# Kernel optimization log

Measured on AMD Instinct MI355X. Metric: run time of the kernel, lower is better.

The kernel has to match this reference:

```python
import jax, jax.numpy as jnp
import numpy as np


def setup_inputs() -> dict:
    key = jax.random.key(0)
    k1, k2 = jax.random.split(key, 2)
    N, H, W, FIN = 64, 64, 64, 64
    FH, FW, FOUT = 4, 4, 128
    L = (H // FH) * (W // FW)  # 256 output locations (stride == kernel)
    X = jax.random.normal(k1, (N, H, W, FIN), dtype=jnp.float32)
    # 'alexnet' init: normal(0, 0.01), unshared per-location filters
    filters = 0.01 * jax.random.normal(k2, (1, L, FH, FW, FIN, FOUT), dtype=jnp.float32)
    bias = jnp.zeros((FOUT,), dtype=jnp.float32)  # bias init value 0.0
    return {"X": X, "filters": filters, "bias": bias}


def reference(X, filters, bias):
    N, H, W, C = X.shape
    _, L, fh, fw, fin, fout = filters.shape
    rows, cols = H // fh, W // fw
    # image_to_patches (stride==kernel branch): non-overlapping patch extraction
    # patches[n, r*cols+c, i, j, ch] = X[n, r*fh+i, c*fw+j, ch]
    patches = X.reshape(N, rows, fh, cols, fw, C)
    patches = patches.transpose(0, 1, 3, 2, 4, 5).reshape(N, L, fh, fw, C)
    # broadcast-multiply + reduce_sum over (fh, fw, fin) == per-location GEMM
    Z = jnp.einsum('nlijc,lijcf->nlf', patches, filters[0]) + bias
    Z = Z.reshape(N, rows, cols, fout)
    return jax.nn.relu(Z)
```

## Files before the change

kernel.cpp:

```cpp
#include <hip/hip_runtime.h>


typedef __bf16 bf16x8 __attribute__((ext_vector_type(8)));
typedef float f32x4 __attribute__((ext_vector_type(4)));

#define SBP 140

__device__ __forceinline__ unsigned pack2(float a, float b) {
  __bf16 lo = (__bf16)a, hi = (__bf16)b;
  return (unsigned)__builtin_bit_cast(unsigned short, lo) |
         ((unsigned)__builtin_bit_cast(unsigned short, hi) << 16);
}

__global__ __launch_bounds__(512) void bioconv_full(
    const float* __restrict__ X, const float* __restrict__ Fw,
    const float* __restrict__ bias, float* __restrict__ out) {
  const int bx = blockIdx.x;
  const int l = (bx & 7) * 32 + (bx >> 3);
  const int r = l >> 4, c = l & 15;

  const int t = threadIdx.x;
  const int wave = t >> 6, lane = t & 63;
  const int q = lane >> 4, nl = lane & 15;
  const int m0 = (wave >> 1) * 16;
  const int n0 = (wave & 1) * 64;

  __shared__ __align__(16) unsigned short As[2][64 * 128];
  __shared__ __align__(16) unsigned Bs[2][64 * SBP];

  const float* gA = X + r * 16384 + c * 256;
  const float* gB = Fw + (size_t)l * 131072;

  float2 vA[8];
  float4 vB0[4], vB1[4];

  auto loadA = [&](int s) {
    const int off = (s >> 1) * 4096 + (s & 1) * 128 + 2 * lane;
#pragma unroll
    for (int m = 0; m < 8; ++m) {
      const int n = m * 8 + wave;
      vA[m] = *(const float2*)(gA + (size_t)n * 262144 + off);
    }
  };
  auto loadB = [&](int s) {
    const float* base = gB + s * 16384 + 4 * (lane & 31);
#pragma unroll
    for (int m = 0; m < 4; ++m) {
      const int kp = wave * 8 + m * 2 + (lane >> 5);
      vB0[m] = *(const float4*)(base + kp * 256);
      vB1[m] = *(const float4*)(base + kp * 256 + 128);
    }
  };
  auto writeA = [&](int buf) {
    unsigned* base = (unsigned*)&As[buf][0];
#pragma unroll
    for (int m = 0; m < 8; ++m) {
      const int n = m * 8 + wave;
      base[n * 64 + (lane ^ ((n & 7) << 2))] = pack2(vA[m].x, vA[m].y);
    }
  };
  auto writeB = [&](int buf) {
    unsigned* bw = (unsigned*)&Bs[buf][0] + 4 * (lane & 31);
#pragma unroll
    for (int m = 0; m < 4; ++m) {
      const int kp = wave * 8 + m * 2 + (lane >> 5);
      uint4 v;
      v.x = pack2(vB0[m].x, vB1[m].x);
      v.y = pack2(vB0[m].y, vB1[m].y);
      v.z = pack2(vB0[m].z, vB1[m].z);
      v.w = pack2(vB0[m].w, vB1[m].w);
      *(uint4*)(bw + kp * SBP) = v;
    }
  };

  f32x4 acc[4];
#pragma unroll
  for (int fb = 0; fb < 4; ++fb) acc[fb] = (f32x4){0.f, 0.f, 0.f, 0.f};

  auto compute = [&](int buf) {
#pragma unroll
    for (int kk = 0; kk < 4; ++kk) {
      const unsigned short* ap =
          &As[buf][(m0 + nl) * 128 + ((kk * 32 + q * 8) ^ ((nl & 7) << 3))];
      bf16x8 af = *(const bf16x8*)ap;
      const unsigned* bp = (const unsigned*)&Bs[buf][0] + (kk * 16 + q * 4) * SBP + n0 + nl;
#pragma unroll
      for (int fb = 0; fb < 4; ++fb) {
        const unsigned* b = bp + fb * 16;
        uint4 v;
        v.x = b[0];
        v.y = b[SBP];
        v.z = b[2 * SBP];
        v.w = b[3 * SBP];
        bf16x8 bfr = __builtin_bit_cast(bf16x8, v);
        acc[fb] = __builtin_amdgcn_mfma_f32_16x16x32_bf16(af, bfr, acc[fb], 0, 0, 0);
      }
    }
  };

  loadA(0);
  loadB(0);
  writeA(0);
  writeB(0);
  loadA(1);
  loadB(1);
#pragma unroll
  for (int s = 0; s < 8; ++s) {
    asm volatile("s_waitcnt lgkmcnt(0)" ::: "memory");
    __builtin_amdgcn_s_barrier();
    __builtin_amdgcn_sched_barrier(0);
    compute(s & 1);
    if (s + 1 < 8) {
      writeA((s + 1) & 1);
      writeB((s + 1) & 1);
    }
    if (s + 2 < 8) {
      loadA(s + 2);
      loadB(s + 2);
    }
  }

#pragma unroll
  for (int fb = 0; fb < 4; ++fb) {
    const int f = n0 + fb * 16 + nl;
    const float bv = bias[f];
    float* ob = out + (size_t)l * 128 + f;
#pragma unroll
    for (int v = 0; v < 4; ++v) {
      const int row = m0 + q * 4 + v;
      ob[(size_t)row * 32768] = fmaxf(acc[fb][v] + bv, 0.f);
    }
  }
}

extern "C" void kernel_launch(void* const* d_in, const int* in_sizes, int n_in,
                              void* d_out, int out_size, void* d_ws, size_t ws_size,
                              hipStream_t stream) {
  const float* X = (const float*)d_in[0];
  const float* Fw = (const float*)d_in[1];
  const float* bias = (const float*)d_in[2];
  float* out = (float*)d_out;
  bioconv_full<<<256, 512, 0, stream>>>(X, Fw, bias, out);
}
```

Before: 241.9 us.

## Stream fp32 tiles into LDS via direct global-to-LDS loads with triple buffering

Replaces the register-staged load/convert/write path with global_load_lds DMA that copies fp32 tiles of X and filters straight into LDS, using XOR swizzles and a three-stage buffer ring with vmcnt-based waits. The bf16 conversion moves into the compute loop, done when fragments are read from LDS. This is meant to cut register pressure and VALU/LDS-write work in the load phase and to overlap memory better. In exchange it doubles LDS footprint per stage (fp32 instead of bf16), uses more LDS reads and scalar B reads, and repeats the conversion per wave.

```diff
diff --git a/kernel.cpp b/kernel.cpp
--- a/kernel.cpp
+++ b/kernel.cpp
@@ -4,15 +4,27 @@
 typedef __bf16 bf16x8 __attribute__((ext_vector_type(8)));
 typedef float f32x4 __attribute__((ext_vector_type(4)));
 
-#define SBP 140
-
 __device__ __forceinline__ unsigned pack2(float a, float b) {
   __bf16 lo = (__bf16)a, hi = (__bf16)b;
   return (unsigned)__builtin_bit_cast(unsigned short, lo) |
          ((unsigned)__builtin_bit_cast(unsigned short, hi) << 16);
 }
+__device__ __forceinline__ bf16x8 cvt8(float4 lo, float4 hi) {
+  uint4 v;
+  v.x = pack2(lo.x, lo.y);
+  v.y = pack2(lo.z, lo.w);
+  v.z = pack2(hi.x, hi.y);
+  v.w = pack2(hi.z, hi.w);
+  return __builtin_bit_cast(bf16x8, v);
+}
 
-__global__ __launch_bounds__(512) void bioconv_full(
+__device__ __forceinline__ void gl2lds16(const float* g, float* l) {
+  __builtin_amdgcn_global_load_lds(
+      (const __attribute__((address_space(1))) void*)g,
+      (__attribute__((address_space(3))) void*)l, 16, 0, 0);
+}
+
+__global__ __launch_bounds__(512) void bioconv_dma(
     const float* __restrict__ X, const float* __restrict__ Fw,
     const float* __restrict__ bias, float* __restrict__ out) {
   const int bx = blockIdx.x;
@@ -25,51 +37,33 @@
   const int m0 = (wave >> 1) * 16;
   const int n0 = (wave & 1) * 64;
 
-  __shared__ __align__(16) unsigned short As[2][64 * 128];
-  __shared__ __align__(16) unsigned Bs[2][64 * SBP];
+  __shared__ __align__(16) float Als[3][64 * 64];
+  __shared__ __align__(16) float Bls[3][64 * 128];
 
   const float* gA = X + r * 16384 + c * 256;
   const float* gB = Fw + (size_t)l * 131072;
 
-  float2 vA[8];
-  float4 vB0[4], vB1[4];
+  const int arow_lo = lane >> 4;
+  const int achk = lane & 15;
+  const int brow_lo = lane >> 5;
+  const int bchk = lane & 31;
 
-  auto loadA = [&](int s) {
-    const int off = (s >> 1) * 4096 + (s & 1) * 128 + 2 * lane;
+  auto issueA = [&](int s, int buf) {
 #pragma unroll
-    for (int m = 0; m < 8; ++m) {
-      const int n = m * 8 + wave;
-      vA[m] = *(const float2*)(gA + (size_t)n * 262144 + off);
+    for (int j = 0; j < 2; ++j) {
+      const int row = wave * 8 + j * 4 + arow_lo;
+      const int cg = achk ^ (row & 7);
+      const float* g = gA + (size_t)row * 262144 + (s >> 2) * 4096 + (s & 3) * 64 + cg * 4;
+      gl2lds16(g, &Als[buf][(wave * 8 + j * 4) * 64]);
     }
   };
-  auto loadB = [&](int s) {
-    const float* base = gB + s * 16384 + 4 * (lane & 31);
+  auto issueB = [&](int s, int buf) {
 #pragma unroll
-    for (int m = 0; m < 4; ++m) {
-      const int kp = wave * 8 + m * 2 + (lane >> 5);
-      vB0[m] = *(const float4*)(base + kp * 256);
-      vB1[m] = *(const float4*)(base + kp * 256 + 128);
-    }
-  };
-  auto writeA = [&](int buf) {
-    unsigned* base = (unsigned*)&As[buf][0];
-#pragma unroll
-    for (int m = 0; m < 8; ++m) {
-      const int n = m * 8 + wave;
-      base[n * 64 + (lane ^ ((n & 7) << 2))] = pack2(vA[m].x, vA[m].y);
-    }
-  };
-  auto writeB = [&](int buf) {
-    unsigned* bw = (unsigned*)&Bs[buf][0] + 4 * (lane & 31);
-#pragma unroll
-    for (int m = 0; m < 4; ++m) {
-      const int kp = wave * 8 + m * 2 + (lane >> 5);
-      uint4 v;
-      v.x = pack2(vB0[m].x, vB1[m].x);
-      v.y = pack2(vB0[m].y, vB1[m].y);
-      v.z = pack2(vB0[m].z, vB1[m].z);
-      v.w = pack2(vB0[m].w, vB1[m].w);
-      *(uint4*)(bw + kp * SBP) = v;
+    for (int i = 0; i < 4; ++i) {
+      const int row = i * 16 + wave * 2 + brow_lo;
+      const int cswz = bchk ^ (((row >> 3) & 3) << 2);
+      const float* g = gB + (size_t)(s * 64 + row) * 128 + cswz * 4;
+      gl2lds16(g, &Bls[buf][(i * 16 + wave * 2) * 128]);
     }
   };
 
@@ -78,46 +72,46 @@
   for (int fb = 0; fb < 4; ++fb) acc[fb] = (f32x4){0.f, 0.f, 0.f, 0.f};
 
   auto compute = [&](int buf) {
+    const float* Ab = &Als[buf][0];
+    const float* Bb = &Bls[buf][0];
 #pragma unroll
-    for (int kk = 0; kk < 4; ++kk) {
-      const unsigned short* ap =
-          &As[buf][(m0 + nl) * 128 + ((kk * 32 + q * 8) ^ ((nl & 7) << 3))];
-      bf16x8 af = *(const bf16x8*)ap;
-      const unsigned* bp = (const unsigned*)&Bs[buf][0] + (kk * 16 + q * 4) * SBP + n0 + nl;
+    for (int kk = 0; kk < 2; ++kk) {
+      const int cg = kk * 8 + q * 2;
+      const int w0 = (m0 + nl) * 64 + ((cg + 0) ^ (nl & 7)) * 4;
+      const int w1 = (m0 + nl) * 64 + ((cg + 1) ^ (nl & 7)) * 4;
+      float4 a0 = *(const float4*)(Ab + w0);
+      float4 a1 = *(const float4*)(Ab + w1);
+      bf16x8 af = cvt8(a0, a1);
 #pragma unroll
       for (int fb = 0; fb < 4; ++fb) {
-        const unsigned* b = bp + fb * 16;
-        uint4 v;
-        v.x = b[0];
-        v.y = b[SBP];
-        v.z = b[2 * SBP];
-        v.w = b[3 * SBP];
-        bf16x8 bfr = __builtin_bit_cast(bf16x8, v);
+        const int fw = (n0 + fb * 16 + nl) ^ (q << 4);
+        const float* bp = Bb + (kk * 32 + q * 8) * 128 + fw;
+        float b0 = bp[0 * 128], b1 = bp[1 * 128], b2 = bp[2 * 128], b3 = bp[3 * 128];
+        float b4 = bp[4 * 128], b5 = bp[5 * 128], b6 = bp[6 * 128], b7 = bp[7 * 128];
+        bf16x8 bfr = cvt8(make_float4(b0, b1, b2, b3), make_float4(b4, b5, b6, b7));
         acc[fb] = __builtin_amdgcn_mfma_f32_16x16x32_bf16(af, bfr, acc[fb], 0, 0, 0);
       }
     }
   };
 
-  loadA(0);
-  loadB(0);
-  writeA(0);
-  writeB(0);
-  loadA(1);
-  loadB(1);
+  issueA(0, 0);
+  issueB(0, 0);
+  issueA(1, 1);
+  issueB(1, 1);
+
 #pragma unroll
-  for (int s = 0; s < 8; ++s) {
-    asm volatile("s_waitcnt lgkmcnt(0)" ::: "memory");
+  for (int s = 0; s < 16; ++s) {
+    if (s < 15)
+      asm volatile("s_waitcnt vmcnt(6)" ::: "memory");
+    else
+      asm volatile("s_waitcnt vmcnt(0)" ::: "memory");
     __builtin_amdgcn_s_barrier();
     __builtin_amdgcn_sched_barrier(0);
-    compute(s & 1);
-    if (s + 1 < 8) {
-      writeA((s + 1) & 1);
-      writeB((s + 1) & 1);
+    if (s + 2 < 16) {
+      issueA(s + 2, (s + 2) % 3);
+      issueB(s + 2, (s + 2) % 3);
     }
-    if (s + 2 < 8) {
-      loadA(s + 2);
-      loadB(s + 2);
-    }
+    compute(s % 3);
   }
 
 #pragma unroll
@@ -140,5 +134,5 @@
   const float* Fw = (const float*)d_in[1];
   const float* bias = (const float*)d_in[2];
   float* out = (float*)d_out;
-  bioconv_full<<<256, 512, 0, stream>>>(X, Fw, bias, out);
+  bioconv_dma<<<256, 512, 0, stream>>>(X, Fw, bias, out);
 }
```

New measurement: 241.6 us. Within noise of the previous version (-0.1%).
